# Kernel optimization log

Hardware: AMD Instinct MI355X
Metric: run time of the kernel (lower is better)

The kernel has to match this reference:

```python
import jax, jax.numpy as jnp
import numpy as np

N_QUBITS = 11
DIM = 2 ** N_QUBITS
GAIN = 2 ** 0.5
LRMUL = 1.0
W_MUL = GAIN * 5 ** (-0.5) * LRMUL  # use_wscale=True path


def _build_unitary(weight):
    """Overall circuit unitary. Per qubit q the circuit applies rx, ry, rz
    (left_to_right composition => Rz @ Ry @ Rx on that qubit's subspace).
    Gates on distinct qubits commute, so the sequential product of expanded
    gates equals the kron over qubits of the per-qubit composite 2x2 gate,
    with qubit 0 as the leftmost kron factor (matches gate_expand_1toN)."""
    w = (weight * W_MUL).reshape(N_QUBITS, 3)
    half = w / 2
    c = jnp.cos(half)
    s = jnp.sin(half)
    cx, sx = c[:, 0], s[:, 0]
    cy, sy = c[:, 1], s[:, 1]
    ez = jnp.exp(-1j * half[:, 2])  # e^{-i phi_z / 2}
    zeros = jnp.zeros_like(ez)
    # [n, 2, 2] gate stacks (complex64)
    rx = jnp.stack([jnp.stack([cx + 0j, -1j * sx], -1),
                    jnp.stack([-1j * sx, cx + 0j], -1)], -2)
    ry = jnp.stack([jnp.stack([cy + 0j, -sy + 0j], -1),
                    jnp.stack([sy + 0j, cy + 0j], -1)], -2)
    rz = jnp.stack([jnp.stack([ez, zeros], -1),
                    jnp.stack([zeros, jnp.conj(ez)], -1)], -2)
    g = rz @ ry @ rx  # [n, 2, 2] composite per-qubit gate
    U = g[0]
    for q in range(1, N_QUBITS):  # loop over fixed small n_qubits is fine
        U = jnp.kron(U, g[q])
    return U  # [DIM, DIM] complex64


def setup_inputs() -> dict:
    key = jax.random.key(0)
    kx, kw = jax.random.split(key)
    x = jax.random.normal(kx, (DIM, DIM), dtype=jnp.float32)
    weight = jax.random.uniform(kw, (N_QUBITS * 3,), dtype=jnp.float32,
                                minval=0.0, maxval=2.0 * np.pi)
    return {"x": x, "weight": weight}


def reference(x, weight):
    U = _build_unitary(weight)
    xc = x.astype(jnp.complex64)
    # queryQ_out = U @ x @ U^dagger
    return U @ xc @ jnp.conj(U).T
```

## Files before the change

kernel.cpp:

```cpp
#include <hip/hip_runtime.h>
#include <hip/hip_fp16.h>


#define DIM 2048
#define NQ 11

typedef float v2f __attribute__((ext_vector_type(2)));

__device__ __forceinline__ int swz(int j) { return j ^ ((j >> 5) & 31); }

__device__ __forceinline__ float2 cmul(float2 a, float2 b) {
    return make_float2(a.x * b.x - a.y * b.y, a.x * b.y + a.y * b.x);
}

__device__ __forceinline__ v2f pkmul_swap(v2f s, v2f g) {
    v2f d;
    asm("v_pk_mul_f32 %0, %1, %2 op_sel:[1,0] op_sel_hi:[0,1]"
        : "=v"(d) : "v"(s), "v"(g));
    return d;
}
__device__ __forceinline__ v2f pkfma(v2f s0, v2f s1, v2f c) {
    v2f d;
    asm("v_pk_fma_f32 %0, %1, %2, %3" : "=v"(d) : "v"(s0), "v"(s1), "v"(c));
    return d;
}
__device__ __forceinline__ v2f pkfma_swap(v2f s0, v2f s1, v2f c) {
    v2f d;
    asm("v_pk_fma_f32 %0, %1, %2, %3 op_sel:[1,0,0] op_sel_hi:[0,1,1]"
        : "=v"(d) : "v"(s0), "v"(s1), "v"(c));
    return d;
}

struct PkGate {
    v2f x00, y00, x01, y01, x10, y10, x11, y11;
};

__device__ __forceinline__ void make_gate(const float* __restrict__ w, int q,
                                          int conj, float2* out4) {
    const float WM = 0.632455532033675866f;
    float hx = 0.5f * WM * w[q * 3 + 0];
    float hy = 0.5f * WM * w[q * 3 + 1];
    float hz = 0.5f * WM * w[q * 3 + 2];
    float cx, sx, cy, sy, cz, sz;
    sincosf(hx, &sx, &cx);
    sincosf(hy, &sy, &cy);
    sincosf(hz, &sz, &cz);
    float2 m00 = make_float2(cy * cx,  sy * sx);
    float2 m01 = make_float2(-sy * cx, -cy * sx);
    float2 m10 = make_float2(sy * cx,  -cy * sx);
    float2 m11 = make_float2(cy * cx,  -sy * sx);
    float2 ez  = make_float2(cz, -sz);
    float2 ezc = make_float2(cz,  sz);
    float2 g00 = cmul(ez, m00);
    float2 g01 = cmul(ez, m01);
    float2 g10 = cmul(ezc, m10);
    float2 g11 = cmul(ezc, m11);
    float sgn = conj ? -1.f : 1.f;
    out4[0] = make_float2(g00.x, sgn * g00.y);
    out4[1] = make_float2(g01.x, sgn * g01.y);
    out4[2] = make_float2(g10.x, sgn * g10.y);
    out4[3] = make_float2(g11.x, sgn * g11.y);
}

__device__ __forceinline__ void build_pk_gates(const float* __restrict__ wt,
                                               int t, int conj,
                                               v2f (*gsh)[8]) {
    if (t < NQ) {
        float2 e[4];
        make_gate(wt, t, conj, e);
#pragma unroll
        for (int k = 0; k < 4; ++k) {
            v2f px = {e[k].x, e[k].x};
            v2f py = {-e[k].y, e[k].y};
            gsh[t][2 * k + 0] = px;
            gsh[t][2 * k + 1] = py;
        }
    }
}

__device__ __forceinline__ void load_pkgate(const v2f (*gsh)[8], int q,
                                            PkGate& G) {
    G.x00 = gsh[q][0]; G.y00 = gsh[q][1];
    G.x01 = gsh[q][2]; G.y01 = gsh[q][3];
    G.x10 = gsh[q][4]; G.y10 = gsh[q][5];
    G.x11 = gsh[q][6]; G.y11 = gsh[q][7];
}

__device__ __forceinline__ void bfly(float2& A, float2& B, const PkGate& G) {
    v2f a = __builtin_bit_cast(v2f, A), b = __builtin_bit_cast(v2f, B);
    v2f t;
    t = pkmul_swap(b, G.y01);
    t = pkfma(b, G.x01, t);
    t = pkfma_swap(a, G.y00, t);
    A = __builtin_bit_cast(float2, pkfma(a, G.x00, t));
    t = pkmul_swap(b, G.y11);
    t = pkfma(b, G.x11, t);
    t = pkfma_swap(a, G.y10, t);
    B = __builtin_bit_cast(float2, pkfma(a, G.x10, t));
}

template <int ST>
__device__ __forceinline__ void stage16(float2* v, const PkGate& G) {
#pragma unroll
    for (int m = 0; m < 16; ++m)
        if (!(m & ST)) bfly(v[m], v[m + ST], G);
}

__device__ __forceinline__ unsigned pack_h2(float2 v) {
    __half2 h = __float22half2_rn(v);
    return *reinterpret_cast<unsigned*>(&h);
}
__device__ __forceinline__ float2 unpack_h2(unsigned u) {
    __half2 h = *reinterpret_cast<__half2*>(&u);
    return __half22float2(h);
}

__global__ __launch_bounds__(256, 2) void rowpassK1(
    const float* __restrict__ X, unsigned* __restrict__ Y,
    const float* __restrict__ wt) {
    __shared__ float pRe[2 * DIM];
    __shared__ float pIm[2 * DIM];
    __shared__ v2f gsh[NQ][8];
    int t = threadIdx.x;
    build_pk_gates(wt, t, 1, gsh);
    __syncthreads();

    int u = t & 127, rv = t >> 7;
    int base = rv * DIM;
    int row = blockIdx.x * 2 + rv;
    const float* xrow = X + (size_t)row * DIM;

    float xr[16];
#pragma unroll
    for (int m = 0; m < 16; ++m) xr[m] = xrow[u + (m << 7)];

    float e00x = gsh[3][0][0], e00y = gsh[3][1][1];
    float e01x = gsh[3][2][0], e01y = gsh[3][3][1];
    float e10x = gsh[3][4][0], e10y = gsh[3][5][1];
    float e11x = gsh[3][6][0], e11y = gsh[3][7][1];
    float2 v[16];
#pragma unroll
    for (int m = 0; m < 16; m += 2) {
        float a = xr[m], b = xr[m + 1];
        v[m]     = make_float2(e00x * a + e01x * b, e00y * a + e01y * b);
        v[m + 1] = make_float2(e10x * a + e11x * b, e10y * a + e11y * b);
    }
    PkGate G;
    load_pkgate(gsh, 2, G); stage16<2>(v, G);
    load_pkgate(gsh, 1, G); stage16<4>(v, G);
    load_pkgate(gsh, 0, G); stage16<8>(v, G);

#pragma unroll
    for (int m = 0; m < 16; ++m) {
        int a = base + swz(u + (m << 7));
        pRe[a] = v[m].x; pIm[a] = v[m].y;
    }
    __syncthreads();

    int uLo = u & 7, uHi = u >> 3;
#pragma unroll
    for (int m = 0; m < 16; ++m) {
        int a = base + swz(uLo + (m << 3) + (uHi << 7));
        v[m] = make_float2(pRe[a], pIm[a]);
    }
    load_pkgate(gsh, 7, G); stage16<1>(v, G);
    load_pkgate(gsh, 6, G); stage16<2>(v, G);
    load_pkgate(gsh, 5, G); stage16<4>(v, G);
    load_pkgate(gsh, 4, G); stage16<8>(v, G);
#pragma unroll
    for (int m = 0; m < 16; ++m) {
        int a = base + swz(uLo + (m << 3) + (uHi << 7));
        pRe[a] = v[m].x; pIm[a] = v[m].y;
    }
    __syncthreads();

#pragma unroll
    for (int m = 0; m < 16; ++m) {
        int a = base + swz(m + (u << 4));
        v[m] = make_float2(pRe[a], pIm[a]);
    }
    load_pkgate(gsh, 10, G); stage16<1>(v, G);
    load_pkgate(gsh, 9, G);  stage16<2>(v, G);
    load_pkgate(gsh, 8, G);  stage16<4>(v, G);

    unsigned* yp = Y + (size_t)(2 * u) * (DIM * 8) + (size_t)row * 8;
    uint4 pk0, pk1;
    pk0.x = pack_h2(v[0]); pk0.y = pack_h2(v[1]);
    pk0.z = pack_h2(v[2]); pk0.w = pack_h2(v[3]);
    pk1.x = pack_h2(v[4]); pk1.y = pack_h2(v[5]);
    pk1.z = pack_h2(v[6]); pk1.w = pack_h2(v[7]);
    *reinterpret_cast<uint4*>(yp) = pk0;
    *reinterpret_cast<uint4*>(yp + 4) = pk1;
    unsigned* yp2 = yp + DIM * 8;
    pk0.x = pack_h2(v[8]);  pk0.y = pack_h2(v[9]);
    pk0.z = pack_h2(v[10]); pk0.w = pack_h2(v[11]);
    pk1.x = pack_h2(v[12]); pk1.y = pack_h2(v[13]);
    pk1.z = pack_h2(v[14]); pk1.w = pack_h2(v[15]);
    *reinterpret_cast<uint4*>(yp2) = pk0;
    *reinterpret_cast<uint4*>(yp2 + 4) = pk1;
}

__global__ __launch_bounds__(1024, 4) void colfused(
    const unsigned* __restrict__ Y, float* __restrict__ Out,
    const float* __restrict__ wt, int writeComplex) {
    __shared__ unsigned pk[DIM * 9];
    __shared__ v2f gsh[NQ][8];
    int t = threadIdx.x;
    build_pk_gates(wt, t, 0, gsh);
    __syncthreads();

    int strip = ((blockIdx.x & 7) << 5) + (blockIdx.x >> 3);

    int c = t & 7, u = t >> 3;
    const unsigned* yb = Y + (size_t)strip * (DIM * 8);

    float2 v[16];
    PkGate G;
#pragma unroll
    for (int m = 0; m < 16; ++m)
        v[m] = unpack_h2(yb[(u + (m << 7)) * 8 + c]);

    load_pkgate(gsh, 3, G); stage16<1>(v, G);
    load_pkgate(gsh, 2, G); stage16<2>(v, G);
    load_pkgate(gsh, 1, G); stage16<4>(v, G);
    load_pkgate(gsh, 0, G); stage16<8>(v, G);

#pragma unroll
    for (int m = 0; m < 16; ++m)
        pk[(u + (m << 7)) * 9 + c] = pack_h2(v[m]);
    __syncthreads();

    int uLo = u & 7, uHi = u >> 3;
#pragma unroll
    for (int m = 0; m < 16; ++m)
        v[m] = unpack_h2(pk[(uLo + (m << 3) + (uHi << 7)) * 9 + c]);
    load_pkgate(gsh, 7, G); stage16<1>(v, G);
    load_pkgate(gsh, 6, G); stage16<2>(v, G);
    load_pkgate(gsh, 5, G); stage16<4>(v, G);
    load_pkgate(gsh, 4, G); stage16<8>(v, G);
#pragma unroll
    for (int m = 0; m < 16; ++m)
        pk[(uLo + (m << 3) + (uHi << 7)) * 9 + c] = pack_h2(v[m]);
    __syncthreads();

#pragma unroll
    for (int m = 0; m < 16; ++m)
        v[m] = unpack_h2(pk[(m + (u << 4)) * 9 + c]);
    load_pkgate(gsh, 10, G); stage16<1>(v, G);
    load_pkgate(gsh, 9, G);  stage16<2>(v, G);
    load_pkgate(gsh, 8, G);  stage16<4>(v, G);

    int j = strip * 8 + c;
    if (!writeComplex) {
#pragma unroll
        for (int m = 0; m < 16; ++m)
            Out[(size_t)(m + (u << 4)) * DIM + j] = v[m].x;
    } else {
        float2* o2 = (float2*)Out;
#pragma unroll
        for (int m = 0; m < 16; ++m)
            o2[(size_t)(m + (u << 4)) * DIM + j] = v[m];
    }
}

extern "C" void kernel_launch(void* const* d_in, const int* in_sizes, int n_in,
                              void* d_out, int out_size, void* d_ws,
                              size_t ws_size, hipStream_t stream) {
    const float* X = (const float*)d_in[0];
    const float* wt = (const float*)d_in[1];
    float* out = (float*)d_out;
    unsigned* Y = (unsigned*)d_ws;

    rowpassK1<<<DIM / 2, 256, 0, stream>>>(X, Y, wt);
    int wc = (out_size >= 2 * DIM * DIM) ? 1 : 0;
    colfused<<<DIM / 8, 1024, 0, stream>>>(Y, out, wt, wc);
}
```

Before: 36.45 us.

## Replace shared-memory row transposes with wave-level shuffle butterflies

The row pass now assigns one wavefront per row. Each lane holds 32 elements, and the low six qubit stages are applied across lanes with shuffle-xor exchanges instead of staging data through shared memory with block barriers. The real-input first-stage shortcut is dropped, so all 11 gates run on complex values. The output is written as scalar 32-bit stores instead of uint4 vectors. This removes LDS traffic and __syncthreads, at the cost of many cross-lane shuffles, extra arithmetic and narrower global stores.

```diff
diff --git a/kernel.cpp b/kernel.cpp
--- a/kernel.cpp
+++ b/kernel.cpp
@@ -6,8 +6,6 @@
 #define NQ 11
 
 typedef float v2f __attribute__((ext_vector_type(2)));
-
-__device__ __forceinline__ int swz(int j) { return j ^ ((j >> 5) & 31); }
 
 __device__ __forceinline__ float2 cmul(float2 a, float2 b) {
     return make_float2(a.x * b.x - a.y * b.y, a.x * b.y + a.y * b.x);
@@ -106,6 +104,13 @@
         if (!(m & ST)) bfly(v[m], v[m + ST], G);
 }
 
+template <int ST>
+__device__ __forceinline__ void stage32(float2* v, const PkGate& G) {
+#pragma unroll
+    for (int m = 0; m < 32; ++m)
+        if (!(m & ST)) bfly(v[m], v[m + ST], G);
+}
+
 __device__ __forceinline__ unsigned pack_h2(float2 v) {
     __half2 h = __float22half2_rn(v);
     return *reinterpret_cast<unsigned*>(&h);
@@ -115,89 +120,54 @@
     return __half22float2(h);
 }
 
-__global__ __launch_bounds__(256, 2) void rowpassK1(
+__global__ __launch_bounds__(256, 2) void rowwaveK1(
     const float* __restrict__ X, unsigned* __restrict__ Y,
     const float* __restrict__ wt) {
-    __shared__ float pRe[2 * DIM];
-    __shared__ float pIm[2 * DIM];
     __shared__ v2f gsh[NQ][8];
     int t = threadIdx.x;
     build_pk_gates(wt, t, 1, gsh);
     __syncthreads();
 
-    int u = t & 127, rv = t >> 7;
-    int base = rv * DIM;
-    int row = blockIdx.x * 2 + rv;
+    int l = t & 63;
+    int row = blockIdx.x * 4 + (t >> 6);
     const float* xrow = X + (size_t)row * DIM;
 
-    float xr[16];
-#pragma unroll
-    for (int m = 0; m < 16; ++m) xr[m] = xrow[u + (m << 7)];
-
-    float e00x = gsh[3][0][0], e00y = gsh[3][1][1];
-    float e01x = gsh[3][2][0], e01y = gsh[3][3][1];
-    float e10x = gsh[3][4][0], e10y = gsh[3][5][1];
-    float e11x = gsh[3][6][0], e11y = gsh[3][7][1];
-    float2 v[16];
-#pragma unroll
-    for (int m = 0; m < 16; m += 2) {
-        float a = xr[m], b = xr[m + 1];
-        v[m]     = make_float2(e00x * a + e01x * b, e00y * a + e01y * b);
-        v[m + 1] = make_float2(e10x * a + e11x * b, e10y * a + e11y * b);
+    float2 v[32];
+#pragma unroll
+    for (int m = 0; m < 32; ++m)
+        v[m] = make_float2(xrow[l + (m << 6)], 0.f);
+
+#pragma unroll
+    for (int b = 0; b < 6; ++b) {
+        PkGate G;
+        load_pkgate(gsh, 10 - b, G);
+        bool hi = (l >> b) & 1;
+        v2f s0x = hi ? G.x11 : G.x00, s0y = hi ? G.y11 : G.y00;
+        v2f s1x = hi ? G.x10 : G.x01, s1y = hi ? G.y10 : G.y01;
+#pragma unroll
+        for (int m = 0; m < 32; ++m) {
+            v2f pv;
+            pv[0] = __shfl_xor(v[m].x, 1 << b);
+            pv[1] = __shfl_xor(v[m].y, 1 << b);
+            v2f a = __builtin_bit_cast(v2f, v[m]);
+            v2f tt = pkmul_swap(pv, s1y);
+            tt = pkfma(pv, s1x, tt);
+            tt = pkfma_swap(a, s0y, tt);
+            v[m] = __builtin_bit_cast(float2, pkfma(a, s0x, tt));
+        }
     }
+
     PkGate G;
-    load_pkgate(gsh, 2, G); stage16<2>(v, G);
-    load_pkgate(gsh, 1, G); stage16<4>(v, G);
-    load_pkgate(gsh, 0, G); stage16<8>(v, G);
-
-#pragma unroll
-    for (int m = 0; m < 16; ++m) {
-        int a = base + swz(u + (m << 7));
-        pRe[a] = v[m].x; pIm[a] = v[m].y;
-    }
-    __syncthreads();
-
-    int uLo = u & 7, uHi = u >> 3;
-#pragma unroll
-    for (int m = 0; m < 16; ++m) {
-        int a = base + swz(uLo + (m << 3) + (uHi << 7));
-        v[m] = make_float2(pRe[a], pIm[a]);
-    }
-    load_pkgate(gsh, 7, G); stage16<1>(v, G);
-    load_pkgate(gsh, 6, G); stage16<2>(v, G);
-    load_pkgate(gsh, 5, G); stage16<4>(v, G);
-    load_pkgate(gsh, 4, G); stage16<8>(v, G);
-#pragma unroll
-    for (int m = 0; m < 16; ++m) {
-        int a = base + swz(uLo + (m << 3) + (uHi << 7));
-        pRe[a] = v[m].x; pIm[a] = v[m].y;
-    }
-    __syncthreads();
-
-#pragma unroll
-    for (int m = 0; m < 16; ++m) {
-        int a = base + swz(m + (u << 4));
-        v[m] = make_float2(pRe[a], pIm[a]);
-    }
-    load_pkgate(gsh, 10, G); stage16<1>(v, G);
-    load_pkgate(gsh, 9, G);  stage16<2>(v, G);
-    load_pkgate(gsh, 8, G);  stage16<4>(v, G);
-
-    unsigned* yp = Y + (size_t)(2 * u) * (DIM * 8) + (size_t)row * 8;
-    uint4 pk0, pk1;
-    pk0.x = pack_h2(v[0]); pk0.y = pack_h2(v[1]);
-    pk0.z = pack_h2(v[2]); pk0.w = pack_h2(v[3]);
-    pk1.x = pack_h2(v[4]); pk1.y = pack_h2(v[5]);
-    pk1.z = pack_h2(v[6]); pk1.w = pack_h2(v[7]);
-    *reinterpret_cast<uint4*>(yp) = pk0;
-    *reinterpret_cast<uint4*>(yp + 4) = pk1;
-    unsigned* yp2 = yp + DIM * 8;
-    pk0.x = pack_h2(v[8]);  pk0.y = pack_h2(v[9]);
-    pk0.z = pack_h2(v[10]); pk0.w = pack_h2(v[11]);
-    pk1.x = pack_h2(v[12]); pk1.y = pack_h2(v[13]);
-    pk1.z = pack_h2(v[14]); pk1.w = pack_h2(v[15]);
-    *reinterpret_cast<uint4*>(yp2) = pk0;
-    *reinterpret_cast<uint4*>(yp2 + 4) = pk1;
+    load_pkgate(gsh, 4, G); stage32<1>(v, G);
+    load_pkgate(gsh, 3, G); stage32<2>(v, G);
+    load_pkgate(gsh, 2, G); stage32<4>(v, G);
+    load_pkgate(gsh, 1, G); stage32<8>(v, G);
+    load_pkgate(gsh, 0, G); stage32<16>(v, G);
+
+    unsigned* yp = Y + (size_t)(l >> 3) * (DIM * 8) + (size_t)row * 8 + (l & 7);
+#pragma unroll
+    for (int m = 0; m < 32; ++m)
+        yp[(size_t)m * 8 * (DIM * 8)] = pack_h2(v[m]);
 }
 
 __global__ __launch_bounds__(1024, 4) void colfused(
@@ -271,7 +241,7 @@
     float* out = (float*)d_out;
     unsigned* Y = (unsigned*)d_ws;
 
-    rowpassK1<<<DIM / 2, 256, 0, stream>>>(X, Y, wt);
+    rowwaveK1<<<DIM / 4, 256, 0, stream>>>(X, Y, wt);
     int wc = (out_size >= 2 * DIM * DIM) ? 1 : 0;
     colfused<<<DIM / 8, 1024, 0, stream>>>(Y, out, wt, wc);
 }
```

New measurement: 43.46 us. +19.2%, slower.
